# Optimization experiments

Hardware: AMD Instinct MI355X
Metric: run time of the kernel (lower is better)

## Reference

```python
import jax, jax.numpy as jnp
import numpy as np

EMB_W, COMMIT_W, ENT_W = 1.0, 0.25, 0.1  # loss weights from init_kwargs


def setup_inputs() -> dict:
    key = jax.random.key(0)
    k1, k2 = jax.random.split(key)
    B, H, W, D, K = 32, 32, 32, 64, 1024
    inputs = jax.random.normal(k1, (B, H, W, D), dtype=jnp.float32)
    # keras RandomUniform default: U(-0.05, 0.05)
    codebook = jax.random.uniform(k2, (K, D), dtype=jnp.float32, minval=-0.05, maxval=0.05)
    return {"inputs": inputs, "codebook": codebook}


def reference(inputs, codebook):
    # inputs: [B,H,W,D], codebook: [K,D]
    D = inputs.shape[-1]
    x = inputs.reshape(-1, D)  # [N,D]
    dist = (
        jnp.sum(x * x, axis=-1, keepdims=True)
        - 2.0 * (x @ codebook.T)
        + jnp.sum(codebook * codebook, axis=-1)
    )  # [N,K]
    tokens = jnp.argmin(dist, axis=-1)  # [N]
    emb = codebook[tokens].reshape(inputs.shape)  # [B,H,W,D]

    embedding_loss = EMB_W * jnp.mean((jax.lax.stop_gradient(emb) - inputs) ** 2)
    commitment_loss = COMMIT_W * jnp.mean((emb - jax.lax.stop_gradient(inputs)) ** 2)
    # 'entropy' loss as written in call(): mean over codebook of per-code min distance
    entropy_loss = ENT_W * jnp.mean(jnp.min(dist, axis=0))
    loss = embedding_loss + commitment_loss + entropy_loss

    # training=True path: straight-through estimator
    out = inputs + jax.lax.stop_gradient(emb - inputs)
    return out, loss
```

## Files before the change

kernel.cpp:

```cpp
#include <hip/hip_runtime.h>
#include <math.h>

#define NROWS 32768
#define NCODE 1024
#define AMB_CAP 8192
#define GAP_THRESH 1.5e-4f

typedef __attribute__((ext_vector_type(8))) short bf16x8;
typedef __attribute__((ext_vector_type(4))) float f32x4;

__device__ __forceinline__ unsigned short bf16_rne(float f) {
    unsigned u = __float_as_uint(f);
    unsigned r = u + 0x7FFFu + ((u >> 16) & 1u);
    return (unsigned short)(r >> 16);
}

typedef const __attribute__((address_space(1))) unsigned GU;
typedef __attribute__((address_space(3))) unsigned LU;
__device__ __forceinline__ void gl_lds16(const void* g, void* l) {
    __builtin_amdgcn_global_load_lds((GU*)g, (LU*)l, 16, 0, 0);
}
__device__ __forceinline__ void gl_lds4(const void* g, void* l) {
    __builtin_amdgcn_global_load_lds((GU*)g, (LU*)l, 4, 0, 0);
}

__global__ __launch_bounds__(64) void vq_prep(
    const float* __restrict__ cb, float* __restrict__ cn4,
    unsigned* __restrict__ minK, unsigned* __restrict__ counter,
    float* __restrict__ gsumsq, unsigned* __restrict__ ticket,
    unsigned short* __restrict__ wsB)
{
    int c = blockIdx.x * 64 + threadIdx.x;
    if (c == 0) { *counter = 0u; *gsumsq = 0.f; *ticket = 0u; }
    float v[64];
    const float4* src = (const float4*)(cb + (size_t)c * 64);
    float s = 0.f;
    #pragma unroll
    for (int i = 0; i < 16; i++) {
        float4 t = src[i];
        v[i*4+0] = t.x; v[i*4+1] = t.y; v[i*4+2] = t.z; v[i*4+3] = t.w;
        s += t.x*t.x + t.y*t.y + t.z*t.z + t.w*t.w;
    }
    cn4[c] = s + 4.0f;
    minK[c] = 0x7F800000u;
    int cc = c >> 6, ct = (c >> 4) & 3, cl = c & 15;
    #pragma unroll
    for (int q = 0; q < 4; q++) {
        int half = q & 1, lo = q >> 1;
        #pragma unroll
        for (int g = 0; g < 4; g++) {
            unsigned short u8[8] __attribute__((aligned(16)));
            #pragma unroll
            for (int j = 0; j < 8; j++) {
                float f = v[half*32 + g*8 + j];
                unsigned short h = bf16_rne(f);
                if (lo) h = bf16_rne(f - __uint_as_float((unsigned)h << 16));
                u8[j] = h;
            }
            size_t off = (size_t)cc * 8192 + ct * 2048 + q * 512 + (g * 16 + cl) * 8;
            *(uint4*)(wsB + off) = *(const uint4*)u8;
        }
    }
}

__global__ __launch_bounds__(512, 4) void vq_main(
    const float* __restrict__ x, const float* __restrict__ cb,
    const unsigned short* __restrict__ wsB, const float* __restrict__ cn4,
    float* __restrict__ out, unsigned* __restrict__ minK,
    unsigned* __restrict__ counter, int* __restrict__ amb,
    float* __restrict__ gsumsq)
{
    __shared__ __align__(16) unsigned char Bb[2][32768];
    __shared__ float cn4L[2][128];
    __shared__ unsigned scrE[1024];
    __shared__ float mD1[128], mD2[128];
    __shared__ int   mI1[128];
    __shared__ int   tokS[64];
    __shared__ float redS[8];

    const int tid = threadIdx.x;
    const int lane = tid & 63;
    const int wi = tid >> 6;
    const int g = wi >> 1;
    const int h = wi & 1;
    const int ln15 = lane & 15;
    const int q = lane >> 4;
    const int row0 = blockIdx.x * 64;
    const int rot = blockIdx.x & 7;

    scrE[tid] = 0x7F800000u;
    scrE[512 + tid] = 0x7F800000u;

    const char* wsBb = (const char*)wsB;
    {
        int wbase = (tid & ~63) * 16;
        #pragma unroll
        for (int i = 0; i < 4; i++)
            gl_lds16(wsBb + (size_t)rot*32768 + (i*512 + tid)*16,
                     (void*)&Bb[0][i*8192 + wbase]);
        if (wi == 0) {
            gl_lds4(cn4 + rot*128 + lane,      (void*)&cn4L[0][0]);
            gl_lds4(cn4 + rot*128 + 64 + lane, (void*)&cn4L[0][64]);
        }
    }

    bf16x8 Ah0, Ah1, Al0, Al1;
    float xnm4[4];
    {
        const float* xr = x + (size_t)(row0 + g*16 + ln15) * 64 + q * 8;
        float4 f0 = *(const float4*)xr;
        float4 f1 = *(const float4*)(xr + 4);
        float4 f2 = *(const float4*)(xr + 32);
        float4 f3 = *(const float4*)(xr + 36);
        float fa[8] = {f0.x,f0.y,f0.z,f0.w,f1.x,f1.y,f1.z,f1.w};
        float fb[8] = {f2.x,f2.y,f2.z,f2.w,f3.x,f3.y,f3.z,f3.w};
        unsigned short hh8[8] __attribute__((aligned(16)));
        unsigned short ll8[8] __attribute__((aligned(16)));
        unsigned short h28[8] __attribute__((aligned(16)));
        unsigned short l28[8] __attribute__((aligned(16)));
        float ss = 0.f;
        #pragma unroll
        for (int j = 0; j < 8; j++) {
            ss += fa[j]*fa[j] + fb[j]*fb[j];
            unsigned short hh = bf16_rne(fa[j]);
            hh8[j] = hh; ll8[j] = bf16_rne(fa[j] - __uint_as_float((unsigned)hh << 16));
            hh = bf16_rne(fb[j]);
            h28[j] = hh; l28[j] = bf16_rne(fb[j] - __uint_as_float((unsigned)hh << 16));
        }
        Ah0 = *(const bf16x8*)hh8; Al0 = *(const bf16x8*)ll8;
        Ah1 = *(const bf16x8*)h28; Al1 = *(const bf16x8*)l28;
        ss += __shfl_xor(ss, 16);
        ss += __shfl_xor(ss, 32);
        #pragma unroll
        for (int r = 0; r < 4; r++)
            xnm4[r] = __shfl(ss, (q << 2) | r, 64) - 4.0f;
    }

    float d1[4], d2[4];
    int   i1[4];
    #pragma unroll
    for (int r = 0; r < 4; r++) { d1[r] = INFINITY; d2[r] = INFINITY; i1[r] = 0; }

    for (int s = 0; s < 8; s++) {
        __syncthreads();
        const int cb_ = s & 1, nb = (s + 1) & 1;
        const int cphys = (s + rot) & 7;
        if (s < 7) {
            const int cnx = (s + 1 + rot) & 7;
            int wbase = (tid & ~63) * 16;
            #pragma unroll
            for (int i = 0; i < 4; i++)
                gl_lds16(wsBb + (size_t)cnx*32768 + (i*512 + tid)*16,
                         (void*)&Bb[nb][i*8192 + wbase]);
            if (wi == 0) {
                gl_lds4(cn4 + cnx*128 + lane,      (void*)&cn4L[nb][0]);
                gl_lds4(cn4 + cnx*128 + 64 + lane, (void*)&cn4L[nb][64]);
            }
        }
        const unsigned char* buf = Bb[cb_];
        #pragma unroll
        for (int lct = 0; lct < 4; lct++) {
            const int ct = 4*h + lct;
            const unsigned char* tb = buf + (ct >> 2)*16384 + (ct & 3)*4096;
            bf16x8 Bh0 = *(const bf16x8*)(tb +    0 + lane*16);
            bf16x8 Bh1 = *(const bf16x8*)(tb + 1024 + lane*16);
            bf16x8 Bl0 = *(const bf16x8*)(tb + 2048 + lane*16);
            bf16x8 Bl1 = *(const bf16x8*)(tb + 3072 + lane*16);
            float cn4v = cn4L[cb_][ct*16 + ln15];
            int kid = cphys*128 + ct*16 + ln15;
            f32x4 z = {0.f, 0.f, 0.f, 0.f};
            f32x4 acc0 = __builtin_amdgcn_mfma_f32_16x16x32_bf16(Ah0, Bh0, z, 0, 0, 0);
            f32x4 acc1 = __builtin_amdgcn_mfma_f32_16x16x32_bf16(Ah1, Bh1, z, 0, 0, 0);
            acc0 = __builtin_amdgcn_mfma_f32_16x16x32_bf16(Ah0, Bl0, acc0, 0, 0, 0);
            acc1 = __builtin_amdgcn_mfma_f32_16x16x32_bf16(Ah1, Bl1, acc1, 0, 0, 0);
            acc0 = __builtin_amdgcn_mfma_f32_16x16x32_bf16(Al0, Bh0, acc0, 0, 0, 0);
            acc1 = __builtin_amdgcn_mfma_f32_16x16x32_bf16(Al1, Bh1, acc1, 0, 0, 0);
            float cminv = INFINITY;
            #pragma unroll
            for (int r = 0; r < 4; r++) {
                float sdot = acc0[r] + acc1[r];
                float wv = fmaf(sdot, -2.0f, cn4v);
                bool lt = wv < d1[r];
                d2[r] = lt ? d1[r] : fminf(d2[r], wv);
                i1[r] = lt ? kid   : i1[r];
                d1[r] = lt ? wv    : d1[r];
                cminv = fminf(cminv, wv + xnm4[r]);
            }
            cminv = fminf(cminv, __shfl_xor(cminv, 16));
            cminv = fminf(cminv, __shfl_xor(cminv, 32));
            if (q == lct) atomicMin(&scrE[kid], __float_as_uint(cminv));
        }
    }
    __syncthreads();

    #pragma unroll
    for (int d = 1; d < 16; d <<= 1) {
        #pragma unroll
        for (int r = 0; r < 4; r++) {
            float od1 = __shfl_xor(d1[r], d);
            int   oi1 = __shfl_xor(i1[r], d);
            float od2 = __shfl_xor(d2[r], d);
            bool take = (od1 < d1[r]) || (od1 == d1[r] && oi1 < i1[r]);
            float loser = take ? d1[r] : od1;
            d2[r] = fminf(fminf(d2[r], od2), loser);
            d1[r] = take ? od1 : d1[r];
            i1[r] = take ? oi1 : i1[r];
        }
    }
    if (ln15 == 0) {
        #pragma unroll
        for (int r = 0; r < 4; r++) {
            int idx = (g*16 + q*4 + r) * 2 + h;
            mD1[idx] = d1[r]; mI1[idx] = i1[r]; mD2[idx] = d2[r];
        }
    }
    __syncthreads();

    if (tid < 64) {
        float a1 = mD1[tid*2],   b1 = mD1[tid*2+1];
        int   ai = mI1[tid*2],   bi = mI1[tid*2+1];
        float a2 = mD2[tid*2],   b2 = mD2[tid*2+1];
        bool ta = (a1 < b1) || (a1 == b1 && ai < bi);
        float D1 = ta ? a1 : b1;
        int   I1 = ta ? ai : bi;
        float D2 = ta ? fminf(a2, b1) : fminf(b2, a1);
        tokS[tid] = I1;
        if (D2 - D1 < GAP_THRESH) {
            unsigned idx = atomicAdd(counter, 1u);
            if (idx < AMB_CAP) { amb[2*idx] = row0 + tid; amb[2*idx+1] = I1; }
        }
    }

    {
        unsigned u0 = scrE[tid];
        if (u0 < minK[tid]) atomicMin(&minK[tid], u0);
        unsigned u1 = scrE[512 + tid];
        if (u1 < minK[512 + tid]) atomicMin(&minK[512 + tid], u1);
    }
    __syncthreads();

    {
        float acc2 = 0.f;
        #pragma unroll
        for (int uu = 0; uu < 2; uu++) {
            int u = uu*512 + tid;
            int row = u >> 4, c4 = u & 15;
            int tok = tokS[row];
            float4 c = ((const float4*)(cb + (size_t)tok*64))[c4];
            float4 xx = ((const float4*)(x + (size_t)(row0 + row)*64))[c4];
            ((float4*)(out + (size_t)(row0 + row)*64))[c4] = c;
            float dx = c.x-xx.x, dy = c.y-xx.y, dz = c.z-xx.z, dw = c.w-xx.w;
            acc2 += dx*dx + dy*dy + dz*dz + dw*dw;
        }
        #pragma unroll
        for (int o = 32; o > 0; o >>= 1) acc2 += __shfl_down(acc2, o);
        if (lane == 0) redS[wi] = acc2;
        __syncthreads();
        if (tid == 0) {
            float t = 0.f;
            #pragma unroll
            for (int w = 0; w < 8; w++) t += redS[w];
            atomicAdd(gsumsq, t);
        }
    }
}

__global__ __launch_bounds__(256) void vq_tail(
    const float* __restrict__ x, const float* __restrict__ cb,
    float* __restrict__ out, const unsigned* __restrict__ counter,
    const int* __restrict__ amb, float* __restrict__ gsumsq,
    unsigned* __restrict__ ticket, const unsigned* __restrict__ minK,
    float* __restrict__ out_loss)
{
    __shared__ __align__(16) float cbS[16384];
    __shared__ double xs[64];
    __shared__ double bd[256];
    __shared__ int    bi[256];
    __shared__ unsigned lastS;
    __shared__ float redS[4];

    const int tid = threadIdx.x;

    unsigned cnt = *counter; if (cnt > AMB_CAP) cnt = AMB_CAP;
    for (unsigned i = blockIdx.x; i < cnt; i += gridDim.x) {
        int row = amb[2*i], oldk = amb[2*i+1];
        __syncthreads();
        if (tid < 64) xs[tid] = (double)x[(size_t)row*64 + tid];
        __syncthreads();
        double xn = 0.0;
        #pragma unroll 8
        for (int d = 0; d < 64; d++) xn += xs[d]*xs[d];
        double best = INFINITY; int bk = 1 << 30;
        for (int b = 0; b < 4; b++) {
            __syncthreads();
            #pragma unroll
            for (int k = 0; k < 16; k++)
                ((float4*)cbS)[k*256 + tid] = ((const float4*)cb)[b*4096 + k*256 + tid];
            __syncthreads();
            int kcode = b*256 + tid;
            const int t6 = tid & 63;
            double dot = 0.0, cn2 = 0.0;
            #pragma unroll 8
            for (int dd = 0; dd < 64; dd++) {
                int d = (dd + t6) & 63;
                double cv = (double)cbS[tid*64 + d];
                dot = fma(xs[d], cv, dot);
                cn2 = fma(cv, cv, cn2);
            }
            double dist = (xn - 2.0*dot) + cn2;
            if (dist < best || (dist == best && kcode < bk)) { best = dist; bk = kcode; }
        }
        bd[tid] = best; bi[tid] = bk;
        __syncthreads();
        for (int s = 128; s > 0; s >>= 1) {
            if (tid < s) {
                double od = bd[tid+s]; int ok = bi[tid+s];
                if (od < bd[tid] || (od == bd[tid] && ok < bi[tid])) { bd[tid] = od; bi[tid] = ok; }
            }
            __syncthreads();
        }
        int bestk = bi[0];
        if (bestk != oldk) {
            double part = 0.0;
            if (tid < 64) {
                float cn = cb[(size_t)bestk*64 + tid];
                float co = cb[(size_t)oldk*64 + tid];
                out[(size_t)row*64 + tid] = cn;
                double dn = (double)cn - xs[tid];
                double dl = (double)co - xs[tid];
                part = dn*dn - dl*dl;
            }
            __syncthreads();
            bd[tid] = part;
            __syncthreads();
            for (int s = 128; s > 0; s >>= 1) {
                if (tid < s) bd[tid] += bd[tid+s];
                __syncthreads();
            }
            if (tid == 0) atomicAdd(gsumsq, (float)bd[0]);
        }
    }

    __syncthreads();
    if (tid == 0) {
        __threadfence();
        lastS = (atomicAdd(ticket, 1u) == 63u) ? 1u : 0u;
    }
    __syncthreads();
    if (lastS) {
        __threadfence();
        float s = 0.f;
        #pragma unroll
        for (int jj = 0; jj < 4; jj++)
            s += __uint_as_float(minK[jj*256 + tid]);
        #pragma unroll
        for (int o = 32; o > 0; o >>= 1) s += __shfl_down(s, o);
        if ((tid & 63) == 0) redS[tid >> 6] = s;
        __syncthreads();
        if (tid == 0) {
            float gs = atomicAdd(gsumsq, 0.0f);
            float tot = redS[0] + redS[1] + redS[2] + redS[3];
            out_loss[0] = 1.25f * (gs / 2097152.0f) + 0.1f * (tot / 1024.0f);
        }
    }
}

extern "C" void kernel_launch(void* const* d_in, const int* in_sizes, int n_in,
                              void* d_out, int out_size, void* d_ws, size_t ws_size,
                              hipStream_t stream) {
    const float* x  = (const float*)d_in[0];
    const float* cb = (const float*)d_in[1];
    float* out = (float*)d_out;

    char* ws = (char*)d_ws;
    unsigned*       counter = (unsigned*)ws;
    float*          gsumsq  = (float*)(ws + 4);
    unsigned*       ticket  = (unsigned*)(ws + 8);
    float*          cn4     = (float*)(ws + 1024);
    unsigned*       minK    = (unsigned*)(ws + 8192);
    int*            amb     = (int*)(ws + 16384);
    unsigned short* wsB     = (unsigned short*)(ws + 131072);

    vq_prep<<<16,  64,  0, stream>>>(cb, cn4, minK, counter, gsumsq, ticket, wsB);
    vq_main<<<512, 512, 0, stream>>>(x, cb, wsB, cn4, out, minK, counter, amb, gsumsq);
    vq_tail<<<64,  256, 0, stream>>>(x, cb, out, counter, amb, gsumsq, ticket, minK,
                                     out + 2097152);
}
```

Measured before the change: 113.2 us.

## Stream codebook tiles directly from global memory with a 2x32 rows-by-quarter wave split

```diff
diff --git a/kernel.cpp b/kernel.cpp
--- a/kernel.cpp
+++ b/kernel.cpp
@@ -13,15 +13,6 @@
     unsigned u = __float_as_uint(f);
     unsigned r = u + 0x7FFFu + ((u >> 16) & 1u);
     return (unsigned short)(r >> 16);
-}
-
-typedef const __attribute__((address_space(1))) unsigned GU;
-typedef __attribute__((address_space(3))) unsigned LU;
-__device__ __forceinline__ void gl_lds16(const void* g, void* l) {
-    __builtin_amdgcn_global_load_lds((GU*)g, (LU*)l, 16, 0, 0);
-}
-__device__ __forceinline__ void gl_lds4(const void* g, void* l) {
-    __builtin_amdgcn_global_load_lds((GU*)g, (LU*)l, 4, 0, 0);
 }
 
 __global__ __launch_bounds__(64) void vq_prep(
@@ -52,7 +43,7 @@
             unsigned short u8[8] __attribute__((aligned(16)));
             #pragma unroll
             for (int j = 0; j < 8; j++) {
-                float f = v[half*32 + g*8 + j];
+                float f = -2.0f * v[half*32 + g*8 + j];
                 unsigned short h = bf16_rne(f);
                 if (lo) h = bf16_rne(f - __uint_as_float((unsigned)h << 16));
                 u8[j] = h;
@@ -70,44 +61,32 @@
     unsigned* __restrict__ counter, int* __restrict__ amb,
     float* __restrict__ gsumsq)
 {
-    __shared__ __align__(16) unsigned char Bb[2][32768];
-    __shared__ float cn4L[2][128];
+    __shared__ float    cn4L[1024];
     __shared__ unsigned scrE[1024];
-    __shared__ float mD1[128], mD2[128];
-    __shared__ int   mI1[128];
+    __shared__ float mD1[256], mD2[256];
+    __shared__ int   mI1[256];
     __shared__ int   tokS[64];
     __shared__ float redS[8];
 
     const int tid = threadIdx.x;
     const int lane = tid & 63;
     const int wi = tid >> 6;
-    const int g = wi >> 1;
-    const int h = wi & 1;
+    const int rh = wi >> 2;
+    const int h2 = wi & 3;
     const int ln15 = lane & 15;
     const int q = lane >> 4;
     const int row0 = blockIdx.x * 64;
-    const int rot = blockIdx.x & 7;
-
-    scrE[tid] = 0x7F800000u;
+
+    cn4L[tid]       = cn4[tid];
+    cn4L[512 + tid] = cn4[512 + tid];
+    scrE[tid]       = 0x7F800000u;
     scrE[512 + tid] = 0x7F800000u;
 
-    const char* wsBb = (const char*)wsB;
-    {
-        int wbase = (tid & ~63) * 16;
-        #pragma unroll
-        for (int i = 0; i < 4; i++)
-            gl_lds16(wsBb + (size_t)rot*32768 + (i*512 + tid)*16,
-                     (void*)&Bb[0][i*8192 + wbase]);
-        if (wi == 0) {
-            gl_lds4(cn4 + rot*128 + lane,      (void*)&cn4L[0][0]);
-            gl_lds4(cn4 + rot*128 + 64 + lane, (void*)&cn4L[0][64]);
-        }
-    }
-
-    bf16x8 Ah0, Ah1, Al0, Al1;
-    float xnm4[4];
-    {
-        const float* xr = x + (size_t)(row0 + g*16 + ln15) * 64 + q * 8;
+    bf16x8 AH0[2], AH1[2], AL0[2], AL1[2];
+    float xnm[8];
+    #pragma unroll
+    for (int s = 0; s < 2; s++) {
+        const float* xr = x + (size_t)(row0 + rh*32 + s*16 + ln15) * 64 + q * 8;
         float4 f0 = *(const float4*)xr;
         float4 f1 = *(const float4*)(xr + 4);
         float4 f2 = *(const float4*)(xr + 32);
@@ -127,76 +106,70 @@
             hh = bf16_rne(fb[j]);
             h28[j] = hh; l28[j] = bf16_rne(fb[j] - __uint_as_float((unsigned)hh << 16));
         }
-        Ah0 = *(const bf16x8*)hh8; Al0 = *(const bf16x8*)ll8;
-        Ah1 = *(const bf16x8*)h28; Al1 = *(const bf16x8*)l28;
+        AH0[s] = *(const bf16x8*)hh8; AL0[s] = *(const bf16x8*)ll8;
+        AH1[s] = *(const bf16x8*)h28; AL1[s] = *(const bf16x8*)l28;
         ss += __shfl_xor(ss, 16);
         ss += __shfl_xor(ss, 32);
         #pragma unroll
         for (int r = 0; r < 4; r++)
-            xnm4[r] = __shfl(ss, (q << 2) | r, 64) - 4.0f;
-    }
-
-    float d1[4], d2[4];
-    int   i1[4];
-    #pragma unroll
-    for (int r = 0; r < 4; r++) { d1[r] = INFINITY; d2[r] = INFINITY; i1[r] = 0; }
-
-    for (int s = 0; s < 8; s++) {
-        __syncthreads();
-        const int cb_ = s & 1, nb = (s + 1) & 1;
-        const int cphys = (s + rot) & 7;
-        if (s < 7) {
-            const int cnx = (s + 1 + rot) & 7;
-            int wbase = (tid & ~63) * 16;
-            #pragma unroll
-            for (int i = 0; i < 4; i++)
-                gl_lds16(wsBb + (size_t)cnx*32768 + (i*512 + tid)*16,
-                         (void*)&Bb[nb][i*8192 + wbase]);
-            if (wi == 0) {
-                gl_lds4(cn4 + cnx*128 + lane,      (void*)&cn4L[nb][0]);
-                gl_lds4(cn4 + cnx*128 + 64 + lane, (void*)&cn4L[nb][64]);
-            }
-        }
-        const unsigned char* buf = Bb[cb_];
-        #pragma unroll
-        for (int lct = 0; lct < 4; lct++) {
-            const int ct = 4*h + lct;
-            const unsigned char* tb = buf + (ct >> 2)*16384 + (ct & 3)*4096;
-            bf16x8 Bh0 = *(const bf16x8*)(tb +    0 + lane*16);
-            bf16x8 Bh1 = *(const bf16x8*)(tb + 1024 + lane*16);
-            bf16x8 Bl0 = *(const bf16x8*)(tb + 2048 + lane*16);
-            bf16x8 Bl1 = *(const bf16x8*)(tb + 3072 + lane*16);
-            float cn4v = cn4L[cb_][ct*16 + ln15];
-            int kid = cphys*128 + ct*16 + ln15;
-            f32x4 z = {0.f, 0.f, 0.f, 0.f};
-            f32x4 acc0 = __builtin_amdgcn_mfma_f32_16x16x32_bf16(Ah0, Bh0, z, 0, 0, 0);
-            f32x4 acc1 = __builtin_amdgcn_mfma_f32_16x16x32_bf16(Ah1, Bh1, z, 0, 0, 0);
-            acc0 = __builtin_amdgcn_mfma_f32_16x16x32_bf16(Ah0, Bl0, acc0, 0, 0, 0);
-            acc1 = __builtin_amdgcn_mfma_f32_16x16x32_bf16(Ah1, Bl1, acc1, 0, 0, 0);
-            acc0 = __builtin_amdgcn_mfma_f32_16x16x32_bf16(Al0, Bh0, acc0, 0, 0, 0);
-            acc1 = __builtin_amdgcn_mfma_f32_16x16x32_bf16(Al1, Bh1, acc1, 0, 0, 0);
-            float cminv = INFINITY;
-            #pragma unroll
-            for (int r = 0; r < 4; r++) {
-                float sdot = acc0[r] + acc1[r];
-                float wv = fmaf(sdot, -2.0f, cn4v);
-                bool lt = wv < d1[r];
-                d2[r] = lt ? d1[r] : fminf(d2[r], wv);
-                i1[r] = lt ? kid   : i1[r];
-                d1[r] = lt ? wv    : d1[r];
-                cminv = fminf(cminv, wv + xnm4[r]);
-            }
-            cminv = fminf(cminv, __shfl_xor(cminv, 16));
-            cminv = fminf(cminv, __shfl_xor(cminv, 32));
-            if (q == lct) atomicMin(&scrE[kid], __float_as_uint(cminv));
-        }
-    }
-    __syncthreads();
+            xnm[s*4 + r] = __shfl(ss, (q << 2) | r, 64) - 4.0f;
+    }
+    __syncthreads();
+
+    float d1[8], d2[8];
+    int   i1[8];
+    #pragma unroll
+    for (int r = 0; r < 8; r++) { d1[r] = INFINITY; d2[r] = INFINITY; i1[r] = 0; }
+
+    const char* wsQ = (const char*)wsB + (size_t)h2 * 65536 + lane * 16;
+    #pragma unroll
+    for (int t = 0; t < 16; t++) {
+        const char* tb = wsQ + t * 4096;
+        bf16x8 Bh0 = *(const bf16x8*)(tb);
+        bf16x8 Bh1 = *(const bf16x8*)(tb + 1024);
+        bf16x8 Bl0 = *(const bf16x8*)(tb + 2048);
+        bf16x8 Bl1 = *(const bf16x8*)(tb + 3072);
+        const int kid = h2*256 + t*16 + ln15;
+        const float cn4v = cn4L[kid];
+        f32x4 a0 = {cn4v, cn4v, cn4v, cn4v};
+        f32x4 a1 = a0;
+        a0 = __builtin_amdgcn_mfma_f32_16x16x32_bf16(AH0[0], Bh0, a0, 0, 0, 0);
+        a1 = __builtin_amdgcn_mfma_f32_16x16x32_bf16(AH0[1], Bh0, a1, 0, 0, 0);
+        a0 = __builtin_amdgcn_mfma_f32_16x16x32_bf16(AH1[0], Bh1, a0, 0, 0, 0);
+        a1 = __builtin_amdgcn_mfma_f32_16x16x32_bf16(AH1[1], Bh1, a1, 0, 0, 0);
+        a0 = __builtin_amdgcn_mfma_f32_16x16x32_bf16(AH0[0], Bl0, a0, 0, 0, 0);
+        a1 = __builtin_amdgcn_mfma_f32_16x16x32_bf16(AH0[1], Bl0, a1, 0, 0, 0);
+        a0 = __builtin_amdgcn_mfma_f32_16x16x32_bf16(AH1[0], Bl1, a0, 0, 0, 0);
+        a1 = __builtin_amdgcn_mfma_f32_16x16x32_bf16(AH1[1], Bl1, a1, 0, 0, 0);
+        a0 = __builtin_amdgcn_mfma_f32_16x16x32_bf16(AL0[0], Bh0, a0, 0, 0, 0);
+        a1 = __builtin_amdgcn_mfma_f32_16x16x32_bf16(AL0[1], Bh0, a1, 0, 0, 0);
+        a0 = __builtin_amdgcn_mfma_f32_16x16x32_bf16(AL1[0], Bh1, a0, 0, 0, 0);
+        a1 = __builtin_amdgcn_mfma_f32_16x16x32_bf16(AL1[1], Bh1, a1, 0, 0, 0);
+        float cm = INFINITY;
+        #pragma unroll
+        for (int r = 0; r < 4; r++) {
+            float wv = a0[r];
+            bool lt = wv < d1[r];
+            d2[r] = lt ? d1[r] : fminf(d2[r], wv);
+            i1[r] = lt ? kid   : i1[r];
+            d1[r] = lt ? wv    : d1[r];
+            cm = fminf(cm, wv + xnm[r]);
+            float wu = a1[r];
+            bool lu = wu < d1[4+r];
+            d2[4+r] = lu ? d1[4+r] : fminf(d2[4+r], wu);
+            i1[4+r] = lu ? kid     : i1[4+r];
+            d1[4+r] = lu ? wu      : d1[4+r];
+            cm = fminf(cm, wu + xnm[4+r]);
+        }
+        cm = fminf(cm, __shfl_xor(cm, 16));
+        cm = fminf(cm, __shfl_xor(cm, 32));
+        if (q == (t & 3)) atomicMin(&scrE[kid], __float_as_uint(cm));
+    }
 
     #pragma unroll
     for (int d = 1; d < 16; d <<= 1) {
         #pragma unroll
-        for (int r = 0; r < 4; r++) {
+        for (int r = 0; r < 8; r++) {
             float od1 = __shfl_xor(d1[r], d);
             int   oi1 = __shfl_xor(i1[r], d);
             float od2 = __shfl_xor(d2[r], d);
@@ -210,20 +183,26 @@
     if (ln15 == 0) {
         #pragma unroll
         for (int r = 0; r < 4; r++) {
-            int idx = (g*16 + q*4 + r) * 2 + h;
-            mD1[idx] = d1[r]; mI1[idx] = i1[r]; mD2[idx] = d2[r];
+            int rowA = rh*32 + q*4 + r;
+            mD1[rowA*4 + h2] = d1[r];   mI1[rowA*4 + h2] = i1[r];   mD2[rowA*4 + h2] = d2[r];
+            int rowB = rowA + 16;
+            mD1[rowB*4 + h2] = d1[4+r]; mI1[rowB*4 + h2] = i1[4+r]; mD2[rowB*4 + h2] = d2[4+r];
         }
     }
     __syncthreads();
 
     if (tid < 64) {
-        float a1 = mD1[tid*2],   b1 = mD1[tid*2+1];
-        int   ai = mI1[tid*2],   bi = mI1[tid*2+1];
-        float a2 = mD2[tid*2],   b2 = mD2[tid*2+1];
-        bool ta = (a1 < b1) || (a1 == b1 && ai < bi);
-        float D1 = ta ? a1 : b1;
-        int   I1 = ta ? ai : bi;
-        float D2 = ta ? fminf(a2, b1) : fminf(b2, a1);
+        float D1 = mD1[tid*4]; int I1 = mI1[tid*4]; float D2 = mD2[tid*4];
+        #pragma unroll
+        for (int j = 1; j < 4; j++) {
+            float b1 = mD1[tid*4 + j];
+            int   bi = mI1[tid*4 + j];
+            float b2 = mD2[tid*4 + j];
+            bool ta = (D1 < b1) || (D1 == b1 && I1 < bi);
+            float loser = ta ? b1 : D1;
+            D2 = fminf(fminf(D2, b2), loser);
+            if (!ta) { D1 = b1; I1 = bi; }
+        }
         tokS[tid] = I1;
         if (D2 - D1 < GAP_THRESH) {
             unsigned idx = atomicAdd(counter, 1u);
```

Measured after the change: 190.2 us. 68.0% more time.
